# Performance work log

Measured on AMD Instinct MI355X. Metric: run time of the kernel, lower is better.

Reference implementation:

```python
import jax, jax.numpy as jnp
import numpy as np

MARGIN = 0.2
ENCODER_STRIDE = 320


def setup_inputs() -> dict:
    key = jax.random.key(0)
    k1, k2, k3, k4 = jax.random.split(key, 4)
    B, D, T, NC = 8, 512, 2048, 4096
    student_features = jax.random.normal(k1, (B, D, T), dtype=jnp.float32)
    codebook = jax.random.normal(k2, (NC, D), dtype=jnp.float32)
    teacher_codes = jax.random.randint(k3, (B, T), 0, NC, dtype=jnp.int64)
    lengths = jax.random.randint(k4, (B,), 0, T * ENCODER_STRIDE, dtype=jnp.int64)
    return {
        "student_features": student_features,
        "teacher_codes": teacher_codes,
        "codebook": codebook,
        "lengths": lengths,
    }


def reference(student_features, teacher_codes, codebook, lengths):
    B, D, T = student_features.shape
    # frame-level valid mask: (B, T)
    frame_lengths = lengths // ENCODER_STRIDE
    mask = (jnp.arange(T)[None, :] < frame_lengths[:, None]).astype(student_features.dtype)

    # (B*T, D) flattened student vectors
    z = jnp.transpose(student_features, (0, 2, 1)).reshape(-1, D)

    # Euclidean cdist via ||z||^2 + ||c||^2 - 2 z c^T (matmul form, like torch.cdist)
    sq = (
        jnp.sum(z * z, axis=-1, keepdims=True)
        + jnp.sum(codebook * codebook, axis=-1)[None, :]
        - 2.0 * jnp.einsum("nd,cd->nc", z, codebook)
    )
    dists = jnp.sqrt(jnp.maximum(sq, 1e-12))  # (B*T, num_codes)

    teacher_flat = teacher_codes.reshape(-1)
    rows = jnp.arange(teacher_flat.shape[0])
    pos_dist = dists[rows, teacher_flat]
    # exclude the target code, then min over codebook
    dists_for_neg = dists.at[rows, teacher_flat].set(jnp.inf)
    neg_dist = jnp.min(dists_for_neg, axis=1)

    triplet = jax.nn.relu(pos_dist.reshape(B, T) - neg_dist.reshape(B, T) + MARGIN)
    loss = jnp.sum(triplet * mask) / (jnp.sum(mask) + 1e-8)
    return loss
```

## Files before the change

### kernel.cpp

```cpp
#include <hip/hip_runtime.h>
#include <hip/hip_bf16.h>

typedef float f32x4 __attribute__((ext_vector_type(4)));
typedef int v8i __attribute__((ext_vector_type(8)));

#define NB 8
#define ND 512
#define NT 2048
#define NCODES 4096
#define NM (NB * NT)
#define MARGIN_F 0.2f
#define ENC_STRIDE 320


static __device__ inline bool rank_decode(const int* __restrict__ lengths, int rank,
                                          int shift, int& b, int& tib) {
    int acc = 0;
    bool ok = false;
#pragma unroll
    for (int bb = 0; bb < NB; bb++) {
        int fl = lengths[bb] / ENC_STRIDE;
        int c = (fl + ((1 << shift) - 1)) >> shift;
        if (!ok && rank < acc + c) { b = bb; tib = rank - acc; ok = true; }
        acc += c;
    }
    return ok;
}

__global__ void prep_fused(const float* __restrict__ sf, const float* __restrict__ cb,
                           const int* __restrict__ lengths,
                           unsigned char* __restrict__ Zq, float* __restrict__ npart,
                           unsigned char* __restrict__ Cq, float* __restrict__ cnorm,
                           float* __restrict__ accum, unsigned int* __restrict__ ticket) {
    __shared__ float tile[128][65];
    __shared__ float redc[4][16];
    __shared__ float rnp[4][64];
    const int tid = threadIdx.x;
    const int wave = tid >> 6, lane = tid & 63, l15 = lane & 15, kq = lane >> 4;

    if (blockIdx.x < 1024) {
        const int bx = blockIdx.x;
        int b, tt;
        if (!rank_decode(lengths, bx >> 2, 6, b, tt)) return;
        const int t0 = tt * 64;
        const int d0 = (bx & 3) * 128;
        const float* src = sf + (size_t)b * ND * NT;
#pragma unroll
        for (int it = 0; it < 8; it++) {
            int idx = it * 256 + tid;
            int d = idx >> 4, t4 = (idx & 15) * 4;
            float4 v = *(const float4*)(src + (size_t)(d0 + d) * NT + t0 + t4);
            tile[d][t4] = v.x; tile[d][t4 + 1] = v.y; tile[d][t4 + 2] = v.z; tile[d][t4 + 3] = v.w;
        }
        __syncthreads();
        const int m0 = b * NT + t0;
        {
            const int trow = wave * 16 + l15;
            unsigned char q[32];
#pragma unroll
            for (int j = 0; j < 32; j += 2) {
                float a = tile[kq * 32 + j][trow];
                float c = tile[kq * 32 + j + 1][trow];
                int p = __builtin_amdgcn_cvt_pk_fp8_f32(a, c, 0, false);
                q[j] = (unsigned char)(p & 0xFF);
                q[j + 1] = (unsigned char)((p >> 8) & 0xFF);
            }
            const int M_ = m0 >> 7, rg = ((m0 >> 4) & 7) + wave, K_ = d0 >> 7;
            char* base = (char*)Zq + ((size_t)((M_ * 4 + K_) * 8 + rg)) * 2048;
            *(uint4*)(base + lane * 16) = *(uint4*)&q[0];
            *(uint4*)(base + 1024 + lane * 16) = *(uint4*)&q[16];
        }
        {
            const int t = tid & 63, dg = tid >> 6;
            float s = 0.0f;
#pragma unroll 8
            for (int d = 0; d < 32; d++) {
                float v = tile[dg * 32 + d][t];
                s += v * v;
            }
            rnp[dg][t] = s;
            __syncthreads();
            if (tid < 64)
                npart[(size_t)(d0 >> 7) * NM + m0 + tid] =
                    rnp[0][tid] + rnp[1][tid] + rnp[2][tid] + rnp[3][tid];
        }
    } else {
        if (blockIdx.x == 1279 && tid == 0) { *accum = 0.0f; *ticket = 0u; }
        const int r0 = (blockIdx.x - 1024) * 16;
        const int row = r0 + l15;
        const int K_ = wave;
        const float* src = cb + (size_t)row * ND + K_ * 128 + kq * 32;
        unsigned char q[32];
        float s = 0.0f;
#pragma unroll
        for (int j4 = 0; j4 < 8; j4++) {
            float4 v = *(const float4*)(src + j4 * 4);
            s += v.x * v.x + v.y * v.y + v.z * v.z + v.w * v.w;
            int p0 = __builtin_amdgcn_cvt_pk_fp8_f32(v.x, v.y, 0, false);
            int p1 = __builtin_amdgcn_cvt_pk_fp8_f32(v.z, v.w, 0, false);
            q[j4 * 4 + 0] = (unsigned char)(p0 & 0xFF);
            q[j4 * 4 + 1] = (unsigned char)((p0 >> 8) & 0xFF);
            q[j4 * 4 + 2] = (unsigned char)(p1 & 0xFF);
            q[j4 * 4 + 3] = (unsigned char)((p1 >> 8) & 0xFF);
        }
        const int N_ = r0 >> 7, rg = (r0 >> 4) & 7;
        char* base = (char*)Cq + ((size_t)((N_ * 4 + K_) * 8 + rg)) * 2048;
        *(uint4*)(base + lane * 16) = *(uint4*)&q[0];
        *(uint4*)(base + 1024 + lane * 16) = *(uint4*)&q[16];
        s += __shfl_xor(s, 16);
        s += __shfl_xor(s, 32);
        if (lane < 16) redc[wave][l15] = s;
        __syncthreads();
        if (tid < 16) cnorm[r0 + tid] = redc[0][tid] + redc[1][tid] + redc[2][tid] + redc[3][tid];
    }
}

static __device__ inline v8i ldfrag(const char* p) {
    union { uint4 q[2]; v8i v; } u;
    u.q[0] = *(const uint4*)p;
    u.q[1] = *(const uint4*)(p + 1024);
    return u.v;
}

__global__ __launch_bounds__(256, 3) void triplet_main(
    const unsigned char* __restrict__ Zq, const unsigned char* __restrict__ Cq,
    const float* __restrict__ cnorm, const int* __restrict__ teacher,
    const int* __restrict__ lengths,
    float* __restrict__ negq, float* __restrict__ posq) {
    __shared__ float smn[2][64], smp[2][64];

    const int blk = (int)blockIdx.x;
    const int x = blk & 7;
    const int rest = blk >> 3;
    const int N_ = rest & 31;
    const int kk = rest >> 5;
    const int m_rank = x + 8 * kk;
    int b, tM;
    if (!rank_decode(lengths, m_rank, 7, b, tM)) return;
    const int M_ = b * 16 + tM;
    const int m0 = M_ * 128;

    const int tid = threadIdx.x;
    const int wave = tid >> 6, lane = tid & 63;
    const int wr = wave >> 1, wc = wave & 1;
    const int l15 = lane & 15, quad = lane >> 4;

    const float INF = __builtin_inff();
    int tch[4][4];
#pragma unroll
    for (int mi = 0; mi < 4; mi++)
#pragma unroll
        for (int r = 0; r < 4; r++)
            tch[mi][r] = teacher[m0 + wr * 64 + mi * 16 + quad * 4 + r];

    const char* gA = (const char*)Zq + (size_t)(M_ * 4) * 16384 +
                     (size_t)(wr * 4) * 2048 + lane * 16;
    const char* gB = (const char*)Cq + (size_t)(N_ * 4) * 16384 +
                     (size_t)(wc * 4) * 2048 + lane * 16;

    f32x4 acc[4][4];
#pragma unroll
    for (int mi = 0; mi < 4; mi++)
#pragma unroll
        for (int ni = 0; ni < 4; ni++)
            acc[mi][ni] = (f32x4){0.f, 0.f, 0.f, 0.f};

#pragma unroll 1
    for (int kt = 0; kt < 4; ++kt) {
        const char* pA = gA + (size_t)kt * 16384;
        const char* pB = gB + (size_t)kt * 16384;
        v8i av[4], bv[4];
#pragma unroll
        for (int mi = 0; mi < 4; mi++) av[mi] = ldfrag(pA + mi * 2048);
#pragma unroll
        for (int ni = 0; ni < 4; ni++) bv[ni] = ldfrag(pB + ni * 2048);
        __builtin_amdgcn_s_setprio(1);
#pragma unroll
        for (int mi = 0; mi < 4; mi++)
#pragma unroll
            for (int ni = 0; ni < 4; ni++)
                acc[mi][ni] = __builtin_amdgcn_mfma_scale_f32_16x16x128_f8f6f4(
                    av[mi], bv[ni], acc[mi][ni], 0, 0,
                    0, 0x7F7F7F7F, 0, 0x7F7F7F7F);
        __builtin_amdgcn_s_setprio(0);
    }

    const int n0 = N_ * 128;
    float cn[4]; int col[4];
#pragma unroll
    for (int ni = 0; ni < 4; ni++) {
        col[ni] = n0 + wc * 64 + ni * 16 + l15;
        cn[ni] = cnorm[col[ni]];
    }
    float rmn[4][4], rps[4][4];
#pragma unroll
    for (int mi = 0; mi < 4; mi++)
#pragma unroll
        for (int r = 0; r < 4; r++) {
            int t = tch[mi][r];
            float mn = INF, ps = INF;
#pragma unroll
            for (int ni = 0; ni < 4; ni++) {
                float val = fmaf(-2.0f, acc[mi][ni][r], cn[ni]);
                bool ist = (col[ni] == t);
                mn = fminf(mn, ist ? INF : val);
                ps = fminf(ps, ist ? val : INF);
            }
#pragma unroll
            for (int off = 1; off < 16; off <<= 1) {
                mn = fminf(mn, __shfl_xor(mn, off));
                ps = fminf(ps, __shfl_xor(ps, off));
            }
            rmn[mi][r] = mn;
            rps[mi][r] = ps;
        }

    if (wc == 1 && l15 == 0) {
#pragma unroll
        for (int mi = 0; mi < 4; mi++)
#pragma unroll
            for (int r = 0; r < 4; r++) {
                smn[wr][mi * 16 + quad * 4 + r] = rmn[mi][r];
                smp[wr][mi * 16 + quad * 4 + r] = rps[mi][r];
            }
    }
    __syncthreads();
    if (wc == 0 && l15 == 0) {
#pragma unroll
        for (int mi = 0; mi < 4; mi++)
#pragma unroll
            for (int r = 0; r < 4; r++) {
                int rl = mi * 16 + quad * 4 + r;
                float mn = fminf(rmn[mi][r], smn[wr][rl]);
                float ps = fminf(rps[mi][r], smp[wr][rl]);
                int m = m0 + wr * 64 + rl;
                negq[(size_t)N_ * NM + m] = mn;
                posq[(size_t)N_ * NM + m] = ps;
            }
    }
}

__global__ void reduce_final(const float* __restrict__ negq, const float* __restrict__ posq,
                             const float* __restrict__ npart, const int* __restrict__ lengths,
                             float* __restrict__ accum, unsigned int* __restrict__ ticket,
                             float* __restrict__ out) {
    const float INF = __builtin_inff();
    const int t = threadIdx.x & 63;
    const int sg = threadIdx.x >> 6;
    const int m = blockIdx.x * 64 + t;
    float mn = INF, ps = INF;
#pragma unroll
    for (int s = 0; s < 8; s++) {
        mn = fminf(mn, negq[(size_t)(sg * 8 + s) * NM + m]);
        ps = fminf(ps, posq[(size_t)(sg * 8 + s) * NM + m]);
    }
    __shared__ float cmn[4][64], cps[4][64];
    cmn[sg][t] = mn;
    cps[sg][t] = ps;
    __syncthreads();
    if (sg == 0) {
        mn = fminf(fminf(cmn[0][t], cmn[1][t]), fminf(cmn[2][t], cmn[3][t]));
        ps = fminf(fminf(cps[0][t], cps[1][t]), fminf(cps[2][t], cps[3][t]));
        float zn = npart[m] + npart[NM + m] + npart[2 * NM + m] + npart[3 * NM + m];
        float negd = sqrtf(fmaxf(zn + mn, 1e-12f));
        float posd = sqrtf(fmaxf(zn + ps, 1e-12f));
        float tri = fmaxf(posd - negd + MARGIN_F, 0.0f);
        int b = m >> 11;
        int tt = m & (NT - 1);
        int flen = lengths[b] / ENC_STRIDE;
        float val = (tt < flen) ? tri : 0.0f;
#pragma unroll
        for (int off = 1; off < 64; off <<= 1) val += __shfl_xor(val, off);
        if (t == 0) {
            atomicAdd(accum, val);
            __threadfence();
            unsigned int old = atomicAdd(ticket, 1u);
            if (old == 255u) {
                float total = atomicAdd(accum, 0.0f);
                float cnt = 0.0f;
                for (int bb = 0; bb < NB; bb++) cnt += (float)(lengths[bb] / ENC_STRIDE);
                out[0] = total / (cnt + 1e-8f);
            }
        }
    }
}

extern "C" void kernel_launch(void* const* d_in, const int* in_sizes, int n_in,
                              void* d_out, int out_size, void* d_ws, size_t ws_size,
                              hipStream_t stream) {
    const float* sf = (const float*)d_in[0];
    const int* teacher = (const int*)d_in[1];
    const float* cb = (const float*)d_in[2];
    const int* lengths = (const int*)d_in[3];

    char* ws = (char*)d_ws;
    unsigned char* Zq = (unsigned char*)(ws);
    unsigned char* Cq = (unsigned char*)(ws + 8388608);
    float* cnorm = (float*)(ws + 10485760);
    float* npart = (float*)(ws + 10502144);
    float* negq = (float*)(ws + 10764288);
    float* posq = (float*)(ws + 12861440);
    float* accum = (float*)(ws + 14958592);
    unsigned int* ticket = (unsigned int*)(ws + 14958596);

    prep_fused<<<1280, 256, 0, stream>>>(sf, cb, lengths, Zq, npart, Cq, cnorm, accum, ticket);
    triplet_main<<<4096, 256, 0, stream>>>(Zq, Cq, cnorm, teacher, lengths, negq, posq);
    reduce_final<<<256, 256, 0, stream>>>(negq, posq, npart, lengths, accum, ticket,
                                          (float*)d_out);
}
```

Measured before the change: 130.8 us.

## Fuse final reduction into triplet kernel via per-row-tile arrival tickets

Removes the separate reduce_final launch by having the last of the 32 codebook-tile blocks for each 128-row M tile (detected with a per-tile atomic counter) reduce the partial min arrays, compute the triplet loss, and accumulate it. A global ticket counting live row tiles identifies the final block, which writes the normalized loss. This saves a kernel launch and the full pass over all rows, since only valid rows are reduced. In exchange it adds a threadfence and atomics at the end of every main block and a serialized tail on the last-arriving blocks.

```diff
diff --git a/kernel.cpp b/kernel.cpp
--- a/kernel.cpp
+++ b/kernel.cpp
@@ -31,7 +31,8 @@
                            const int* __restrict__ lengths,
                            unsigned char* __restrict__ Zq, float* __restrict__ npart,
                            unsigned char* __restrict__ Cq, float* __restrict__ cnorm,
-                           float* __restrict__ accum, unsigned int* __restrict__ ticket) {
+                           float* __restrict__ accum, unsigned int* __restrict__ ticket,
+                           unsigned int* __restrict__ mtick, float* __restrict__ out) {
     __shared__ float tile[128][65];
     __shared__ float redc[4][16];
     __shared__ float rnp[4][64];
@@ -85,7 +86,10 @@
                     rnp[0][tid] + rnp[1][tid] + rnp[2][tid] + rnp[3][tid];
         }
     } else {
-        if (blockIdx.x == 1279 && tid == 0) { *accum = 0.0f; *ticket = 0u; }
+        if (blockIdx.x == 1279) {
+            if (tid == 0) { *accum = 0.0f; *ticket = 0u; out[0] = 0.0f; }
+            if (tid < 128) mtick[tid] = 0u;
+        }
         const int r0 = (blockIdx.x - 1024) * 16;
         const int row = r0 + l15;
         const int K_ = wave;
@@ -125,9 +129,12 @@
 __global__ __launch_bounds__(256, 3) void triplet_main(
     const unsigned char* __restrict__ Zq, const unsigned char* __restrict__ Cq,
     const float* __restrict__ cnorm, const int* __restrict__ teacher,
-    const int* __restrict__ lengths,
-    float* __restrict__ negq, float* __restrict__ posq) {
+    const int* __restrict__ lengths, const float* __restrict__ npart,
+    float* __restrict__ negq, float* __restrict__ posq,
+    float* __restrict__ accum, unsigned int* __restrict__ ticket,
+    unsigned int* __restrict__ mtick, float* __restrict__ out) {
     __shared__ float smn[2][64], smp[2][64];
+    __shared__ unsigned int lastflag;
 
     const int blk = (int)blockIdx.x;
     const int x = blk & 7;
@@ -238,44 +245,41 @@
                 posq[(size_t)N_ * NM + m] = ps;
             }
     }
-}
-
-__global__ void reduce_final(const float* __restrict__ negq, const float* __restrict__ posq,
-                             const float* __restrict__ npart, const int* __restrict__ lengths,
-                             float* __restrict__ accum, unsigned int* __restrict__ ticket,
-                             float* __restrict__ out) {
-    const float INF = __builtin_inff();
-    const int t = threadIdx.x & 63;
-    const int sg = threadIdx.x >> 6;
-    const int m = blockIdx.x * 64 + t;
-    float mn = INF, ps = INF;
-#pragma unroll
-    for (int s = 0; s < 8; s++) {
-        mn = fminf(mn, negq[(size_t)(sg * 8 + s) * NM + m]);
-        ps = fminf(ps, posq[(size_t)(sg * 8 + s) * NM + m]);
-    }
-    __shared__ float cmn[4][64], cps[4][64];
-    cmn[sg][t] = mn;
-    cps[sg][t] = ps;
+
+    __threadfence();
     __syncthreads();
-    if (sg == 0) {
-        mn = fminf(fminf(cmn[0][t], cmn[1][t]), fminf(cmn[2][t], cmn[3][t]));
-        ps = fminf(fminf(cps[0][t], cps[1][t]), fminf(cps[2][t], cps[3][t]));
-        float zn = npart[m] + npart[NM + m] + npart[2 * NM + m] + npart[3 * NM + m];
-        float negd = sqrtf(fmaxf(zn + mn, 1e-12f));
-        float posd = sqrtf(fmaxf(zn + ps, 1e-12f));
-        float tri = fmaxf(posd - negd + MARGIN_F, 0.0f);
-        int b = m >> 11;
-        int tt = m & (NT - 1);
-        int flen = lengths[b] / ENC_STRIDE;
-        float val = (tt < flen) ? tri : 0.0f;
+    if (tid == 0) lastflag = atomicAdd(&mtick[m_rank], 1u);
+    __syncthreads();
+    if (lastflag == 31u) {
+        float val = 0.0f;
+        if (tid < 128) {
+            const int m = m0 + tid;
+            float mn = INF, ps = INF;
+#pragma unroll 8
+            for (int s = 0; s < 32; s++) {
+                mn = fminf(mn, negq[(size_t)s * NM + m]);
+                ps = fminf(ps, posq[(size_t)s * NM + m]);
+            }
+            float zn = npart[m] + npart[NM + m] + npart[2 * NM + m] + npart[3 * NM + m];
+            float negd = sqrtf(fmaxf(zn + mn, 1e-12f));
+            float posd = sqrtf(fmaxf(zn + ps, 1e-12f));
+            float tri = fmaxf(posd - negd + MARGIN_F, 0.0f);
+            int tt = m & (NT - 1);
+            int flen = lengths[m >> 11] / ENC_STRIDE;
+            val = (tt < flen) ? tri : 0.0f;
+        }
 #pragma unroll
         for (int off = 1; off < 64; off <<= 1) val += __shfl_xor(val, off);
-        if (t == 0) {
-            atomicAdd(accum, val);
+        if ((tid & 63) == 0) smn[0][tid >> 6] = val;
+        __syncthreads();
+        if (tid == 0) {
+            atomicAdd(accum, smn[0][0] + smn[0][1] + smn[0][2] + smn[0][3]);
             __threadfence();
             unsigned int old = atomicAdd(ticket, 1u);
-            if (old == 255u) {
+            int liveR = 0;
+#pragma unroll
+            for (int bb = 0; bb < NB; bb++) liveR += (lengths[bb] / ENC_STRIDE + 127) >> 7;
+            if ((int)old == liveR - 1) {
                 float total = atomicAdd(accum, 0.0f);
                 float cnt = 0.0f;
                 for (int bb = 0; bb < NB; bb++) cnt += (float)(lengths[bb] / ENC_STRIDE);
@@ -302,9 +306,11 @@
     float* posq = (float*)(ws + 12861440);
     float* accum = (float*)(ws + 14958592);
     unsigned int* ticket = (unsigned int*)(ws + 14958596);
-
-    prep_fused<<<1280, 256, 0, stream>>>(sf, cb, lengths, Zq, npart, Cq, cnorm, accum, ticket);
-    triplet_main<<<4096, 256, 0, stream>>>(Zq, Cq, cnorm, teacher, lengths, negq, posq);
-    reduce_final<<<256, 256, 0, stream>>>(negq, posq, npart, lengths, accum, ticket,
-                                          (float*)d_out);
-}
+    unsigned int* mtick = (unsigned int*)(ws + 14958600);
+
+    prep_fused<<<1280, 256, 0, stream>>>(sf, cb, lengths, Zq, npart, Cq, cnorm,
+                                         accum, ticket, mtick, (float*)d_out);
+    triplet_main<<<4096, 256, 0, stream>>>(Zq, Cq, cnorm, teacher, lengths, npart,
+                                           negq, posq, accum, ticket, mtick,
+                                           (float*)d_out);
+}
```

New measurement: 329.1 us. 152% more time.
